# Performance work log

Hardware: AMD Instinct MI355X
Metric: run time of the kernel (lower is better)

## Reference

```python
import jax, jax.numpy as jnp
import numpy as np

HIDDEN = 4096
N_HEADS = 32
N_KV_HEADS = 8
HEAD_DIM = HIDDEN // N_HEADS  # 128
GROUPS = N_HEADS // N_KV_HEADS  # 4
B, S = 1, 2048
NEG = -1e9


def setup_inputs() -> dict:
    key = jax.random.key(0)
    ks = jax.random.split(key, 8)
    hidden_states = jax.random.normal(ks[0], (B, S, HIDDEN), dtype=jnp.float32)
    # additive causal mask [B,1,S,S]
    causal = jnp.tril(jnp.ones((S, S), dtype=bool))
    attention_mask = jnp.where(causal, 0.0, NEG).astype(jnp.float32)[None, None]
    position_ids = jnp.broadcast_to(jnp.arange(S, dtype=jnp.int64), (B, S))
    inv_freq = 1.0 / (500000.0 ** (np.arange(0, HEAD_DIM, 2, dtype=np.float32) / HEAD_DIM))
    freqs = np.arange(S, dtype=np.float32)[:, None] * inv_freq[None, :]  # [S, 64]
    cos = jnp.asarray(np.cos(freqs), dtype=jnp.float32)
    sin = jnp.asarray(np.sin(freqs), dtype=jnp.float32)
    sc = 1.0 / np.sqrt(HIDDEN)
    Wq = jax.random.normal(ks[1], (HIDDEN, HIDDEN), dtype=jnp.float32) * sc
    Wk = jax.random.normal(ks[2], (N_KV_HEADS * HEAD_DIM, HIDDEN), dtype=jnp.float32) * sc
    Wv = jax.random.normal(ks[3], (N_KV_HEADS * HEAD_DIM, HIDDEN), dtype=jnp.float32) * sc
    Wo = jax.random.normal(ks[4], (HIDDEN, HIDDEN), dtype=jnp.float32) * sc
    return {"hidden_states": hidden_states, "attention_mask": attention_mask,
            "position_ids": position_ids, "cos": cos, "sin": sin,
            "Wq": Wq, "Wk": Wk, "Wv": Wv, "Wo": Wo}


def _rope(q, k, cos, sin, position_ids):
    # cos/sin: [max_pos, head_dim//2]; gather per position -> [b,1,s,hd/2]
    c = cos[position_ids][:, None]  # [b,1,s,d/2]
    s_ = sin[position_ids][:, None]
    q1, q2 = q[..., ::2], q[..., 1::2]
    k1, k2 = k[..., ::2], k[..., 1::2]
    q_rot = jnp.concatenate([q1 * c - q2 * s_, q2 * c + q1 * s_], axis=-1)
    k_rot = jnp.concatenate([k1 * c - k2 * s_, k2 * c + k1 * s_], axis=-1)
    return q_rot, k_rot


def reference(hidden_states, attention_mask, position_ids, cos, sin, Wq, Wk, Wv, Wo):
    b, s, _ = hidden_states.shape
    q = jnp.einsum('bsh,oh->bso', hidden_states, Wq).reshape(b, s, N_HEADS, HEAD_DIM).transpose(0, 2, 1, 3)
    k = jnp.einsum('bsh,oh->bso', hidden_states, Wk).reshape(b, s, N_KV_HEADS, HEAD_DIM).transpose(0, 2, 1, 3)
    v = jnp.einsum('bsh,oh->bso', hidden_states, Wv).reshape(b, s, N_KV_HEADS, HEAD_DIM).transpose(0, 2, 1, 3)
    q, k = _rope(q, k, cos, sin, position_ids)
    if GROUPS > 1:
        k = jnp.repeat(k, GROUPS, axis=1)  # [b,H,s,d]
        v = jnp.repeat(v, GROUPS, axis=1)
    scores = jnp.einsum('bhqd,bhkd->bhqk', q, k) / np.sqrt(HEAD_DIM)
    scores = scores + attention_mask
    attn = jax.nn.softmax(scores.astype(jnp.float32), axis=-1).astype(q.dtype)
    out = jnp.einsum('bhqk,bhkd->bhqd', attn, v)
    out = out.transpose(0, 2, 1, 3).reshape(b, s, HIDDEN)
    out = jnp.einsum('bso,ho->bsh', out, Wo)
    return out
```

## Files before the change

kernel.cpp:

```cpp
#include <hip/hip_runtime.h>
#include <hip/hip_bf16.h>

#define S_LEN 2048
#define HID   4096
#define NH    32
#define NKV   8
#define HD    128

typedef __attribute__((ext_vector_type(8))) short short8v;
typedef __attribute__((ext_vector_type(4))) float floatx4;

__device__ __forceinline__ float bf2f(unsigned short u) {
  union { unsigned int u32; float f; } v; v.u32 = ((unsigned int)u) << 16; return v.f;
}
__device__ __forceinline__ unsigned short f2bf(float f) {
  union { float f; unsigned int u; } v; v.f = f;
  unsigned int u = v.u + 0x7fffu + ((v.u >> 16) & 1u);
  return (unsigned short)(u >> 16);
}
__device__ __forceinline__ unsigned int cvtpk_bf16(float lo, float hi) {
  unsigned int r;
  asm("v_cvt_pk_bf16_f32 %0, %1, %2" : "=v"(r) : "v"(lo), "v"(hi));
  return r;
}

__device__ __forceinline__ void gld_lds16(const void* g, void* l) {
  __builtin_amdgcn_global_load_lds((const __attribute__((address_space(1))) void*)g,
                                   (__attribute__((address_space(3))) void*)l, 16, 0, 0);
}

__global__ __launch_bounds__(256) void cvt_all(const float* __restrict__ X,  const float* __restrict__ Wq,
                                               const float* __restrict__ Wk, const float* __restrict__ Wv,
                                               const float* __restrict__ Wo,
                                               unsigned short* __restrict__ Xb,  unsigned short* __restrict__ Wqb,
                                               unsigned short* __restrict__ Wkb, unsigned short* __restrict__ Wvb,
                                               unsigned short* __restrict__ Wob) {
  const int c0 = 2097152;
  const int c1 = c0 + 4194304;
  const int c2 = c1 + 1048576;
  const int c3 = c2 + 1048576;
  const int c4 = c3 + 4194304;
  int i = blockIdx.x * blockDim.x + threadIdx.x;
  int stride = gridDim.x * blockDim.x;
  for (; i < c4; i += stride) {
    const float* src; unsigned short* dst; int off;
    if (i < c0)      { src = X;  dst = Xb;  off = i; }
    else if (i < c1) { src = Wq; dst = Wqb; off = i - c0; }
    else if (i < c2) { src = Wk; dst = Wkb; off = i - c1; }
    else if (i < c3) { src = Wv; dst = Wvb; off = i - c2; }
    else             { src = Wo; dst = Wob; off = i - c3; }
    float4 v = ((const float4*)src)[off];
    ushort4 o;
    o.x = f2bf(v.x); o.y = f2bf(v.y); o.z = f2bf(v.z); o.w = f2bf(v.w);
    ((ushort4*)dst)[off] = o;
  }
}

__device__ __forceinline__ void gemm256_core(const unsigned short* __restrict__ A,
                                             const unsigned short* __restrict__ B,
                                             unsigned short* lds,
                                             int brow, int bcol, int tid,
                                             floatx4 acc[8][4]) {
  const int K = 4096;
  const int w = tid >> 6, lane = tid & 63;
  const int fr = lane & 15, fq = lane >> 4;
  const int wm = w >> 2, wn = w & 3;

  const int r0s = w * 32 + (lane >> 2);
  const int r1s = r0s + 16;
  const int sl0 = ((lane & 3) ^ ((r0s >> 1) & 3)) << 3;
  const int sl1 = ((lane & 3) ^ ((r1s >> 1) & 3)) << 3;
  const unsigned short* pAs0 = A + (size_t)(brow + r0s) * K + sl0;
  const unsigned short* pAs1 = A + (size_t)(brow + r1s) * K + sl1;
  const unsigned short* pBs0 = B + (size_t)(bcol + r0s) * K + sl0;
  const unsigned short* pBs1 = B + (size_t)(bcol + r1s) * K + sl1;

  const int sl = (fq ^ ((fr >> 1) & 3)) << 3;
  int aoffb[8], boffb[4];
#pragma unroll
  for (int m = 0; m < 8; ++m) aoffb[m] = (wm * 128 + m * 16 + fr) * 32 + sl;
#pragma unroll
  for (int n = 0; n < 4; ++n) boffb[n] = 16384 + (wn * 64 + n * 16 + fr) * 32 + sl;

#define STG_A(buf, kh, t)                                                     \
  do {                                                                        \
    const int ko_ = (t) * 64 + (kh) * 32;                                     \
    gld_lds16(pAs0 + ko_, lds + (buf) * 32768 + (kh) * 8192 + w * 1024);      \
    gld_lds16(pAs1 + ko_, lds + (buf) * 32768 + (kh) * 8192 + w * 1024 + 512);\
  } while (0)
#define STG_B(buf, kh, t)                                                     \
  do {                                                                        \
    const int ko_ = (t) * 64 + (kh) * 32;                                     \
    gld_lds16(pBs0 + ko_, lds + (buf) * 32768 + 16384 + (kh) * 8192 + w * 1024);      \
    gld_lds16(pBs1 + ko_, lds + (buf) * 32768 + 16384 + (kh) * 8192 + w * 1024 + 512);\
  } while (0)

  STG_A(0, 0, 0); STG_B(0, 0, 0);
  STG_A(0, 1, 0); STG_B(0, 1, 0);
  STG_A(1, 0, 1); STG_B(1, 0, 1);
  asm volatile("s_waitcnt vmcnt(8)" ::: "memory");
  __builtin_amdgcn_s_barrier();

  const int NT = K / 64;
  for (int t = 0; t < NT; ++t) {
    const int c = t & 1;
    const unsigned short* Lc = lds + c * 32768;
    short8v a_[4], b_[4], a2_[4];

#pragma unroll
    for (int m = 0; m < 4; ++m) a_[m] = *(const short8v*)&Lc[aoffb[m]];
#pragma unroll
    for (int n = 0; n < 4; ++n) b_[n] = *(const short8v*)&Lc[boffb[n]];
    if (t + 1 < NT) STG_A(c ^ 1, 1, t + 1);
    __builtin_amdgcn_s_setprio(1);
#pragma unroll
    for (int m = 0; m < 4; ++m)
#pragma unroll
      for (int n = 0; n < 4; ++n)
        acc[m][n] = __builtin_amdgcn_mfma_f32_16x16x32_bf16(a_[m], b_[n], acc[m][n], 0, 0, 0);
    __builtin_amdgcn_s_setprio(0);
    __builtin_amdgcn_s_barrier();

#pragma unroll
    for (int m = 0; m < 4; ++m) a2_[m] = *(const short8v*)&Lc[aoffb[m + 4]];
    if (t + 1 < NT) STG_B(c ^ 1, 1, t + 1);
    __builtin_amdgcn_s_setprio(1);
#pragma unroll
    for (int m = 0; m < 4; ++m)
#pragma unroll
      for (int n = 0; n < 4; ++n)
        acc[m + 4][n] = __builtin_amdgcn_mfma_f32_16x16x32_bf16(a2_[m], b_[n], acc[m + 4][n], 0, 0, 0);
    __builtin_amdgcn_s_setprio(0);
    if (t == NT - 1) asm volatile("s_waitcnt vmcnt(0)" ::: "memory");
    else             asm volatile("s_waitcnt vmcnt(8)" ::: "memory");
    __builtin_amdgcn_s_barrier();

#pragma unroll
    for (int m = 0; m < 4; ++m) a_[m] = *(const short8v*)&Lc[8192 + aoffb[m]];
#pragma unroll
    for (int n = 0; n < 4; ++n) b_[n] = *(const short8v*)&Lc[8192 + boffb[n]];
    if (t + 2 < NT) STG_A(c, 0, t + 2);
    __builtin_amdgcn_s_setprio(1);
#pragma unroll
    for (int m = 0; m < 4; ++m)
#pragma unroll
      for (int n = 0; n < 4; ++n)
        acc[m][n] = __builtin_amdgcn_mfma_f32_16x16x32_bf16(a_[m], b_[n], acc[m][n], 0, 0, 0);
    __builtin_amdgcn_s_setprio(0);
    __builtin_amdgcn_s_barrier();

#pragma unroll
    for (int m = 0; m < 4; ++m) a2_[m] = *(const short8v*)&Lc[8192 + aoffb[m + 4]];
    if (t + 2 < NT) STG_B(c, 0, t + 2);
    __builtin_amdgcn_s_setprio(1);
#pragma unroll
    for (int m = 0; m < 4; ++m)
#pragma unroll
      for (int n = 0; n < 4; ++n)
        acc[m + 4][n] = __builtin_amdgcn_mfma_f32_16x16x32_bf16(a2_[m], b_[n], acc[m + 4][n], 0, 0, 0);
    __builtin_amdgcn_s_setprio(0);
    if (t >= NT - 2) asm volatile("s_waitcnt vmcnt(0)" ::: "memory");
    else             asm volatile("s_waitcnt vmcnt(8)" ::: "memory");
    __builtin_amdgcn_s_barrier();
  }
#undef STG_A
#undef STG_B
}

__global__ __launch_bounds__(512, 2) void gemm_qkv(const unsigned short* __restrict__ Xb,
                                                   const unsigned short* __restrict__ Wqb,
                                                   const unsigned short* __restrict__ Wkb,
                                                   const unsigned short* __restrict__ Wvb,
                                                   unsigned short* __restrict__ Qg,
                                                   unsigned short* __restrict__ Kg,
                                                   unsigned short* __restrict__ Vt) {
  __shared__ unsigned short lds[2 * 32768];
  const int bx = blockIdx.x;
  const unsigned short* B; unsigned short* C; int mode, bcol, ldc;
  if (bx < 16)      { B = Wqb; C = Qg; mode = 0; bcol = bx * 256;        ldc = HID;  }
  else if (bx < 20) { B = Wkb; C = Kg; mode = 0; bcol = (bx - 16) * 256; ldc = 1024; }
  else              { B = Wvb; C = Vt; mode = 1; bcol = (bx - 20) * 256; ldc = 0;    }
  const int brow = blockIdx.y * 256;
  const int tid = threadIdx.x;
  floatx4 acc[8][4] = {};
  gemm256_core(Xb, B, lds, brow, bcol, tid, acc);

  const int w = tid >> 6, lane = tid & 63;
  const int fr = lane & 15, fq = lane >> 4;
  const int wm = w >> 2, wn = w & 3;
  const int r0 = brow + wm * 128 + fq * 4;
  const int c0 = bcol + wn * 64 + fr;
  if (mode == 0) {
#pragma unroll
    for (int m = 0; m < 8; ++m)
#pragma unroll
      for (int n = 0; n < 4; ++n)
#pragma unroll
        for (int r = 0; r < 4; ++r)
          C[(size_t)(r0 + m * 16 + r) * ldc + c0 + n * 16] = f2bf(acc[m][n][r]);
  } else {
#pragma unroll
    for (int m = 0; m < 8; ++m)
#pragma unroll
      for (int n = 0; n < 4; ++n) {
        ushort4 pk;
        pk.x = f2bf(acc[m][n][0]); pk.y = f2bf(acc[m][n][1]);
        pk.z = f2bf(acc[m][n][2]); pk.w = f2bf(acc[m][n][3]);
        *(ushort4*)&Vt[(size_t)(c0 + n * 16) * S_LEN + (r0 + m * 16)] = pk;
      }
  }
}

__global__ __launch_bounds__(512, 2) void gemm_o(const unsigned short* __restrict__ Ao,
                                                 const unsigned short* __restrict__ Wob,
                                                 float* __restrict__ Out) {
  __shared__ unsigned short lds[2 * 24576];
  const int K = 4096;
  const int tid = threadIdx.x;
  const int w = tid >> 6, lane = tid & 63;
  const int fr = lane & 15, fq = lane >> 4;
  const int wm = w >> 1, wn = w & 1;
  const int brow = blockIdx.y * 256, bcol = blockIdx.x * 128;

  const int rA = tid >> 2;
  const int sA = ((tid & 3) ^ ((rA >> 1) & 3)) << 3;
  const unsigned short* pA0 = Ao  + (size_t)(brow + rA) * K + sA;
  const unsigned short* pA1 = Ao  + (size_t)(brow + 128 + rA) * K + sA;
  const unsigned short* pB0 = Wob + (size_t)(bcol + rA) * K + sA;

  const int sl = (fq ^ ((fr >> 1) & 3)) << 3;
  int aoff[4], boff[4];
#pragma unroll
  for (int m = 0; m < 4; ++m) aoff[m] = (wm * 64 + m * 16 + fr) * 32 + sl;
#pragma unroll
  for (int n = 0; n < 4; ++n) boff[n] = 16384 + (wn * 64 + n * 16 + fr) * 32 + sl;

  floatx4 acc[4][4] = {};

#define STG_KH(buf, kh, t)                                                       \
  do {                                                                           \
    const int ko_ = (t) * 64 + (kh) * 32;                                        \
    gld_lds16(pA0 + ko_, lds + (buf) * 24576 + (kh) * 8192 + w * 512);           \
    gld_lds16(pA1 + ko_, lds + (buf) * 24576 + (kh) * 8192 + 4096 + w * 512);    \
    gld_lds16(pB0 + ko_, lds + (buf) * 24576 + 16384 + (kh) * 4096 + w * 512);   \
  } while (0)

  STG_KH(0, 0, 0);
  STG_KH(0, 1, 0);
  STG_KH(1, 0, 1);
  asm volatile("s_waitcnt vmcnt(6)" ::: "memory");
  __builtin_amdgcn_s_barrier();

  const int NT = K / 64;
  for (int t = 0; t < NT; ++t) {
    const int c = t & 1;
    const unsigned short* Lc = lds + c * 24576;
    short8v a_[4], b_[4];

#pragma unroll
    for (int m = 0; m < 4; ++m) a_[m] = *(const short8v*)&Lc[aoff[m]];
#pragma unroll
    for (int n = 0; n < 4; ++n) b_[n] = *(const short8v*)&Lc[boff[n]];
    if (t + 1 < NT) STG_KH(c ^ 1, 1, t + 1);
    __builtin_amdgcn_s_setprio(1);
#pragma unroll
    for (int m = 0; m < 4; ++m)
#pragma unroll
      for (int n = 0; n < 4; ++n)
        acc[m][n] = __builtin_amdgcn_mfma_f32_16x16x32_bf16(a_[m], b_[n], acc[m][n], 0, 0, 0);
    __builtin_amdgcn_s_setprio(0);
    if (t + 1 < NT) asm volatile("s_waitcnt vmcnt(6)" ::: "memory");
    else            asm volatile("s_waitcnt vmcnt(0)" ::: "memory");
    __builtin_amdgcn_s_barrier();

#pragma unroll
    for (int m = 0; m < 4; ++m) a_[m] = *(const short8v*)&Lc[8192 + aoff[m]];
#pragma unroll
    for (int n = 0; n < 4; ++n) b_[n] = *(const short8v*)&Lc[4096 + boff[n]];
    if (t + 2 < NT) STG_KH(c, 0, t + 2);
    __builtin_amdgcn_s_setprio(1);
#pragma unroll
    for (int m = 0; m < 4; ++m)
#pragma unroll
      for (int n = 0; n < 4; ++n)
        acc[m][n] = __builtin_amdgcn_mfma_f32_16x16x32_bf16(a_[m], b_[n], acc[m][n], 0, 0, 0);
    __builtin_amdgcn_s_setprio(0);
    if (t + 2 < NT)      asm volatile("s_waitcnt vmcnt(6)" ::: "memory");
    else if (t + 1 < NT) asm volatile("s_waitcnt vmcnt(3)" ::: "memory");
    else                 asm volatile("s_waitcnt vmcnt(0)" ::: "memory");
    __builtin_amdgcn_s_barrier();
  }
#undef STG_KH

  const int r0 = brow + wm * 64 + fq * 4;
  const int c0 = bcol + wn * 64 + fr;
#pragma unroll
  for (int m = 0; m < 4; ++m)
#pragma unroll
    for (int n = 0; n < 4; ++n)
#pragma unroll
      for (int r = 0; r < 4; ++r)
        Out[(size_t)(r0 + m * 16 + r) * HID + c0 + n * 16] = acc[m][n][r];
}

__global__ __launch_bounds__(256) void rope_k(const unsigned short* __restrict__ In,
                                              const float* __restrict__ cosT,
                                              const float* __restrict__ sinT,
                                              unsigned short* __restrict__ Out) {
  int idx = blockIdx.x * 256 + threadIdx.x;
  int j = idx & 63;
  int s = (idx >> 6) & (S_LEN - 1);
  int h = idx >> 17;
  unsigned int pr = *(const unsigned int*)(In + (size_t)s * (NKV * HD) + h * HD + 2 * j);
  float k1 = bf2f((unsigned short)(pr & 0xffffu));
  float k2 = bf2f((unsigned short)(pr >> 16));
  float c = cosT[s * 64 + j], sn = sinT[s * 64 + j];
  unsigned int pk = (unsigned int)f2bf(k1 * c - k2 * sn) |
                    ((unsigned int)f2bf(k2 * c + k1 * sn) << 16);
  *(unsigned int*)(Out + ((size_t)h * S_LEN + s) * HD + 2 * j) = pk;
}

__global__ __launch_bounds__(512, 4) void attn_fwd(const unsigned short* __restrict__ Qg,
                                                   const float* __restrict__ cosT,
                                                   const float* __restrict__ sinT,
                                                   const unsigned short* __restrict__ Kr,
                                                   const unsigned short* __restrict__ Vt,
                                                   unsigned short* __restrict__ Ao) {
  __shared__ unsigned short Kl[2][64 * 128];
  __shared__ unsigned short Vl[2][128 * 64];
  const int id = blockIdx.x;
  const int xcd = id & 7, rr = id >> 3;
  const int qt = 15 - (rr >> 2);
  const int h  = xcd * 4 + (rr & 3);
  const int hk = h >> 2;
  const int qb = qt * 128;
  const int tid = threadIdx.x, w = tid >> 6, lane = tid & 63;
  const int fr = lane & 15, fq = lane >> 4;

  short8v aq[4];
  {
    const int s_row = qb + w * 16 + fr;
    const unsigned short* qp = Qg + (size_t)s_row * HID + h * HD + fq * 8;
    const float* cb = cosT + s_row * 64;
    const float* sb = sinT + s_row * 64;
    const float SC = 0.12751744f;
#pragma unroll
    for (int ks = 0; ks < 4; ++ks) {
      short8v raw = *(const short8v*)(qp + ks * 32);
      short8v ov;
#pragma unroll
      for (int e = 0; e < 4; ++e) {
        float q1 = bf2f((unsigned short)raw[2 * e]);
        float q2 = bf2f((unsigned short)raw[2 * e + 1]);
        int j = ks * 16 + fq * 4 + e;
        float c = cb[j], sn = sb[j];
        ov[2 * e]     = (short)f2bf(SC * (q1 * c - q2 * sn));
        ov[2 * e + 1] = (short)f2bf(SC * (q2 * c + q1 * sn));
      }
      aq[ks] = ov;
    }
  }

  const int kcb = ((tid & 15) * 16) ^ (((tid >> 4) & 7) << 4);
  const unsigned short* pK0 = Kr + ((size_t)hk * S_LEN + (tid >> 4)) * HD + (kcb >> 1);
  const int vcb = ((tid & 7) * 16) ^ (((tid >> 3) & 7) << 4);
  const unsigned short* pV0 = Vt + ((size_t)hk * HD + (tid >> 3)) * S_LEN + (vcb >> 1);

  const int hsel = fq >> 1;
  const int srcA = fr + ((2 * (fq & 1)) << 4);
  const int srcB = fr + ((2 * (fq & 1) + 1) << 4);

  float l_acc = 0.f;
  floatx4 o[8] = {};

#define STAGE(buf, t)                                                           \
  do {                                                                          \
    const unsigned short* pk_ = pK0 + (size_t)(t) * 64 * HD;                    \
    const unsigned short* pv_ = pV0 + (t) * 64;                                 \
    _Pragma("unroll")                                                           \
    for (int j = 0; j < 2; ++j)                                                 \
      gld_lds16(pk_ + (size_t)j * 32 * HD, &Kl[buf][j * 4096 + w * 512]);       \
    _Pragma("unroll")                                                           \
    for (int j = 0; j < 2; ++j)                                                 \
      gld_lds16(pv_ + (size_t)j * 64 * S_LEN, &Vl[buf][j * 4096 + w * 512]);    \
  } while (0)

  STAGE(0, 0);
  asm volatile("s_waitcnt vmcnt(0)" ::: "memory");
  __syncthreads();

  const int nt = 2 * qt + 2;
  int cur = 0;
  for (int t = 0; t < nt; ++t) {
    const int kv0 = t * 64;
    if (t + 1 < nt) STAGE(cur ^ 1, t + 1);

    floatx4 St[4] = {};
    const unsigned short* Kc = &Kl[cur][0];
    const unsigned short* Vc = &Vl[cur][0];
    __builtin_amdgcn_s_setprio(1);
#pragma unroll
    for (int ks = 0; ks < 4; ++ks) {
#pragma unroll
      for (int n = 0; n < 4; ++n) {
        int row = n * 16 + fr;
        int cb = (ks * 64 + fq * 16) ^ ((row & 7) << 4);
        short8v kf = *(const short8v*)&Kc[row * 128 + (cb >> 1)];
        St[n] = __builtin_amdgcn_mfma_f32_16x16x32_bf16(kf, aq[ks], St[n], 0, 0, 0);
      }
    }
    __builtin_amdgcn_s_setprio(0);

    if (t >= 2 * qt) {
#pragma unroll
      for (int n = 0; n < 4; ++n) {
#pragma unroll
        for (int r = 0; r < 4; ++r) {
          int kvg = kv0 + n * 16 + fq * 4 + r;
          if (kvg > qb + w * 16 + fr) St[n][r] = -1e30f;
        }
      }
    }

    unsigned int pk[4][2];
#pragma unroll
    for (int n = 0; n < 4; ++n) {
      float p0 = exp2f(St[n][0]);
      float p1 = exp2f(St[n][1]);
      float p2 = exp2f(St[n][2]);
      float p3 = exp2f(St[n][3]);
      l_acc += (p0 + p1) + (p2 + p3);
      pk[n][0] = cvtpk_bf16(p0, p1);
      pk[n][1] = cvtpk_bf16(p2, p3);
    }

    short8v pa[2];
#pragma unroll
    for (int ks = 0; ks < 2; ++ks) {
      unsigned int v0a = __shfl(pk[2 * ks][0], srcA), v0b = __shfl(pk[2 * ks + 1][0], srcA);
      unsigned int v1a = __shfl(pk[2 * ks][1], srcA), v1b = __shfl(pk[2 * ks + 1][1], srcA);
      unsigned int v2a = __shfl(pk[2 * ks][0], srcB), v2b = __shfl(pk[2 * ks + 1][0], srcB);
      unsigned int v3a = __shfl(pk[2 * ks][1], srcB), v3b = __shfl(pk[2 * ks + 1][1], srcB);
      uint4 u;
      u.x = hsel ? v0b : v0a;
      u.y = hsel ? v1b : v1a;
      u.z = hsel ? v2b : v2a;
      u.w = hsel ? v3b : v3a;
      pa[ks] = *(short8v*)&u;
    }

    __builtin_amdgcn_s_setprio(1);
#pragma unroll
    for (int nf = 0; nf < 8; ++nf) {
#pragma unroll
      for (int ks = 0; ks < 2; ++ks) {
        int row = nf * 16 + fr;
        int cb = (ks * 64 + fq * 16) ^ ((row & 7) << 4);
        short8v bv = *(const short8v*)&Vc[row * 64 + (cb >> 1)];
        o[nf] = __builtin_amdgcn_mfma_f32_16x16x32_bf16(pa[ks], bv, o[nf], 0, 0, 0);
      }
    }
    __builtin_amdgcn_s_setprio(0);

    if (t + 1 < nt) {
      asm volatile("s_waitcnt vmcnt(0)" ::: "memory");
      __syncthreads();
      cur ^= 1;
    }
  }
#undef STAGE

  float L = l_acc;
  L += __shfl_xor(L, 16);
  L += __shfl_xor(L, 32);
  float rinv[4];
#pragma unroll
  for (int r = 0; r < 4; ++r) rinv[r] = 1.0f / __shfl(L, fq * 4 + r);

  unsigned short* aop = Ao + (size_t)(qb + w * 16 + fq * 4) * HID + h * HD + fr;
#pragma unroll
  for (int nf = 0; nf < 8; ++nf)
#pragma unroll
    for (int r = 0; r < 4; ++r)
      aop[(size_t)r * HID + nf * 16] = f2bf(o[nf][r] * rinv[r]);
}

extern "C" void kernel_launch(void* const* d_in, const int* in_sizes, int n_in,
                              void* d_out, int out_size, void* d_ws, size_t ws_size,
                              hipStream_t stream) {
  (void)in_sizes; (void)n_in; (void)out_size; (void)ws_size;
  const float* X    = (const float*)d_in[0];
  const float* cosT = (const float*)d_in[3];
  const float* sinT = (const float*)d_in[4];
  const float* Wq   = (const float*)d_in[5];
  const float* Wk   = (const float*)d_in[6];
  const float* Wv   = (const float*)d_in[7];
  const float* Wo   = (const float*)d_in[8];

  char* ws = (char*)d_ws;
  size_t off = 0;
  auto alloc = [&](size_t bytes) { char* p = ws + off; off += (bytes + 255) & ~(size_t)255; return p; };
  unsigned short* Xb  = (unsigned short*)alloc((size_t)S_LEN * HID * 2);
  unsigned short* Wqb = (unsigned short*)alloc((size_t)HID * HID * 2);
  unsigned short* Wkb = (unsigned short*)alloc((size_t)1024 * HID * 2);
  unsigned short* Wvb = (unsigned short*)alloc((size_t)1024 * HID * 2);
  unsigned short* Wob = (unsigned short*)alloc((size_t)HID * HID * 2);
  unsigned short* Qg  = (unsigned short*)alloc((size_t)S_LEN * HID * 2);
  unsigned short* Kg  = (unsigned short*)alloc((size_t)S_LEN * 1024 * 2);
  unsigned short* Vt  = (unsigned short*)alloc((size_t)1024 * S_LEN * 2);
  unsigned short* Kr = Wqb;
  unsigned short* Ao = Xb;

  cvt_all<<<2048, 256, 0, stream>>>(X, Wq, Wk, Wv, Wo, Xb, Wqb, Wkb, Wvb, Wob);
  gemm_qkv<<<dim3(24, 8), 512, 0, stream>>>(Xb, Wqb, Wkb, Wvb, Qg, Kg, Vt);
  rope_k<<<(NKV * S_LEN * 64) / 256, 256, 0, stream>>>(Kg, cosT, sinT, Kr);
  attn_fwd<<<512, 512, 0, stream>>>(Qg, cosT, sinT, Kr, Vt, Ao);
  gemm_o<<<dim3(32, 8), 512, 0, stream>>>(Ao, Wob, (float*)d_out);
}
```

Measured before the change: 293.2 us.

## Merge GEMM half-steps into full k-steps and widen conversion stores

The GEMM main loop now does two phases per 64-wide k tile instead of four. Each phase loads all eight A fragments and issues the A and B prefetches together, which removes two barriers per tile and changes the vmcnt wait accounting. This adds register pressure from eight live A fragments and a coarser load/compute interleave. Separately, the fp32-to-bf16 conversion kernel now processes eight elements per thread with 16-byte stores, halving loop iterations.

```diff
diff --git a/kernel.cpp b/kernel.cpp
--- a/kernel.cpp
+++ b/kernel.cpp
@@ -35,11 +35,11 @@
                                                unsigned short* __restrict__ Xb,  unsigned short* __restrict__ Wqb,
                                                unsigned short* __restrict__ Wkb, unsigned short* __restrict__ Wvb,
                                                unsigned short* __restrict__ Wob) {
-  const int c0 = 2097152;
-  const int c1 = c0 + 4194304;
-  const int c2 = c1 + 1048576;
-  const int c3 = c2 + 1048576;
-  const int c4 = c3 + 4194304;
+  const int c0 = 1048576;
+  const int c1 = c0 + 2097152;
+  const int c2 = c1 + 524288;
+  const int c3 = c2 + 524288;
+  const int c4 = c3 + 2097152;
   int i = blockIdx.x * blockDim.x + threadIdx.x;
   int stride = gridDim.x * blockDim.x;
   for (; i < c4; i += stride) {
@@ -49,10 +49,12 @@
     else if (i < c2) { src = Wk; dst = Wkb; off = i - c1; }
     else if (i < c3) { src = Wv; dst = Wvb; off = i - c2; }
     else             { src = Wo; dst = Wob; off = i - c3; }
-    float4 v = ((const float4*)src)[off];
-    ushort4 o;
-    o.x = f2bf(v.x); o.y = f2bf(v.y); o.z = f2bf(v.z); o.w = f2bf(v.w);
-    ((ushort4*)dst)[off] = o;
+    float4 v0 = ((const float4*)src)[2 * off];
+    float4 v1 = ((const float4*)src)[2 * off + 1];
+    union { ushort4 h[2]; uint4 u; } o;
+    o.h[0].x = f2bf(v0.x); o.h[0].y = f2bf(v0.y); o.h[0].z = f2bf(v0.z); o.h[0].w = f2bf(v0.w);
+    o.h[1].x = f2bf(v1.x); o.h[1].y = f2bf(v1.y); o.h[1].z = f2bf(v1.z); o.h[1].w = f2bf(v1.w);
+    ((uint4*)dst)[off] = o.u;
   }
 }
 
@@ -105,62 +107,39 @@
   for (int t = 0; t < NT; ++t) {
     const int c = t & 1;
     const unsigned short* Lc = lds + c * 32768;
-    short8v a_[4], b_[4], a2_[4];
-
-#pragma unroll
-    for (int m = 0; m < 4; ++m) a_[m] = *(const short8v*)&Lc[aoffb[m]];
+    short8v a_[8], b_[4];
+
+#pragma unroll
+    for (int m = 0; m < 8; ++m) a_[m] = *(const short8v*)&Lc[aoffb[m]];
 #pragma unroll
     for (int n = 0; n < 4; ++n) b_[n] = *(const short8v*)&Lc[boffb[n]];
-    if (t + 1 < NT) STG_A(c ^ 1, 1, t + 1);
-    __builtin_amdgcn_s_setprio(1);
-#pragma unroll
-    for (int m = 0; m < 4; ++m)
+    if (t + 1 < NT) { STG_A(c ^ 1, 1, t + 1); STG_B(c ^ 1, 1, t + 1); }
+    __builtin_amdgcn_s_setprio(1);
+#pragma unroll
+    for (int m = 0; m < 8; ++m)
 #pragma unroll
       for (int n = 0; n < 4; ++n)
         acc[m][n] = __builtin_amdgcn_mfma_f32_16x16x32_bf16(a_[m], b_[n], acc[m][n], 0, 0, 0);
-    __builtin_amdgcn_s_setprio(0);
-    __builtin_amdgcn_s_barrier();
-
-#pragma unroll
-    for (int m = 0; m < 4; ++m) a2_[m] = *(const short8v*)&Lc[aoffb[m + 4]];
-    if (t + 1 < NT) STG_B(c ^ 1, 1, t + 1);
-    __builtin_amdgcn_s_setprio(1);
-#pragma unroll
-    for (int m = 0; m < 4; ++m)
-#pragma unroll
-      for (int n = 0; n < 4; ++n)
-        acc[m + 4][n] = __builtin_amdgcn_mfma_f32_16x16x32_bf16(a2_[m], b_[n], acc[m + 4][n], 0, 0, 0);
     __builtin_amdgcn_s_setprio(0);
     if (t == NT - 1) asm volatile("s_waitcnt vmcnt(0)" ::: "memory");
     else             asm volatile("s_waitcnt vmcnt(8)" ::: "memory");
     __builtin_amdgcn_s_barrier();
 
 #pragma unroll
-    for (int m = 0; m < 4; ++m) a_[m] = *(const short8v*)&Lc[8192 + aoffb[m]];
+    for (int m = 0; m < 8; ++m) a_[m] = *(const short8v*)&Lc[8192 + aoffb[m]];
 #pragma unroll
     for (int n = 0; n < 4; ++n) b_[n] = *(const short8v*)&Lc[8192 + boffb[n]];
-    if (t + 2 < NT) STG_A(c, 0, t + 2);
-    __builtin_amdgcn_s_setprio(1);
-#pragma unroll
-    for (int m = 0; m < 4; ++m)
+    if (t + 2 < NT) { STG_A(c, 0, t + 2); STG_B(c, 0, t + 2); }
+    __builtin_amdgcn_s_setprio(1);
+#pragma unroll
+    for (int m = 0; m < 8; ++m)
 #pragma unroll
       for (int n = 0; n < 4; ++n)
         acc[m][n] = __builtin_amdgcn_mfma_f32_16x16x32_bf16(a_[m], b_[n], acc[m][n], 0, 0, 0);
     __builtin_amdgcn_s_setprio(0);
-    __builtin_amdgcn_s_barrier();
-
-#pragma unroll
-    for (int m = 0; m < 4; ++m) a2_[m] = *(const short8v*)&Lc[8192 + aoffb[m + 4]];
-    if (t + 2 < NT) STG_B(c, 0, t + 2);
-    __builtin_amdgcn_s_setprio(1);
-#pragma unroll
-    for (int m = 0; m < 4; ++m)
-#pragma unroll
-      for (int n = 0; n < 4; ++n)
-        acc[m + 4][n] = __builtin_amdgcn_mfma_f32_16x16x32_bf16(a2_[m], b_[n], acc[m + 4][n], 0, 0, 0);
-    __builtin_amdgcn_s_setprio(0);
-    if (t >= NT - 2) asm volatile("s_waitcnt vmcnt(0)" ::: "memory");
-    else             asm volatile("s_waitcnt vmcnt(8)" ::: "memory");
+    if (t + 2 < NT)      asm volatile("s_waitcnt vmcnt(8)" ::: "memory");
+    else if (t + 1 < NT) asm volatile("s_waitcnt vmcnt(4)" ::: "memory");
+    else                 asm volatile("s_waitcnt vmcnt(0)" ::: "memory");
     __builtin_amdgcn_s_barrier();
   }
 #undef STG_A
```

Measured after the change: 293.9 us. Within noise of the previous version (+0.2%).
